# Kernel tuning notes

Measured on AMD Instinct MI355X. Metric: run time of the kernel, lower is better.

Reference implementation:

```python
import jax, jax.numpy as jnp
import numpy as np

B, L, HID, H, FF = 32, 1024, 512, 8, 2048
DH = HID // H  # head_dim = 64; deterministic FAVOR features => M == DH
KEPS = 1e-3    # performer kernel_epsilon
LN_EPS = 1e-6  # flax LayerNorm default


def setup_inputs() -> dict:
    key = jax.random.key(0)
    ks = jax.random.split(key, 12)
    sa = 1.0 / np.sqrt(HID)
    sf = 1.0 / np.sqrt(FF)
    return {
        "x": jax.random.normal(ks[0], (B, L, HID), jnp.float32),
        "Wq": jax.random.normal(ks[1], (HID, H, DH), jnp.float32) * sa,
        "bq": jnp.zeros((H, DH), jnp.float32),
        "Wk": jax.random.normal(ks[2], (HID, H, DH), jnp.float32) * sa,
        "bk": jnp.zeros((H, DH), jnp.float32),
        "Wv": jax.random.normal(ks[3], (HID, H, DH), jnp.float32) * sa,
        "bv": jnp.zeros((H, DH), jnp.float32),
        "Wo": jax.random.normal(ks[4], (H, DH, HID), jnp.float32) * sa,
        "bo": jnp.zeros((HID,), jnp.float32),
        "ln1_scale": jnp.ones((HID,), jnp.float32),
        "ln1_bias": jnp.zeros((HID,), jnp.float32),
        "W1": jax.random.normal(ks[5], (HID, FF), jnp.float32) * sa,
        "b1": jnp.zeros((FF,), jnp.float32),
        "W2": jax.random.normal(ks[6], (FF, HID), jnp.float32) * sf,
        "b2": jnp.zeros((HID,), jnp.float32),
        "ln2_scale": jnp.ones((HID,), jnp.float32),
        "ln2_bias": jnp.zeros((HID,), jnp.float32),
    }


def _layernorm(x, scale, bias):
    mu = jnp.mean(x, axis=-1, keepdims=True)
    var = jnp.mean(jnp.square(x - mu), axis=-1, keepdims=True)
    return (x - mu) * jax.lax.rsqrt(var + LN_EPS) * scale + bias


def _favor_bidirectional(q, k, v):
    # Performer generalized attention, deterministic features:
    # phi(x) = relu(x) + kernel_epsilon, renormalized.
    qp = jax.nn.relu(q) + KEPS  # [B,L,H,M]
    kp = jax.nn.relu(k) + KEPS  # [B,L,H,M]
    kv = jnp.einsum('blhm,blhd->bhmd', kp, v)        # [B,H,M,D]
    num = jnp.einsum('blhm,bhmd->blhd', qp, kv)      # [B,L,H,D]
    den = jnp.einsum('blhm,bhm->blh', qp, kp.sum(axis=1))  # [B,L,H]
    return num / den[..., None]


def reference(x, Wq, bq, Wk, bk, Wv, bv, Wo, bo,
              ln1_scale, ln1_bias, W1, b1, W2, b2, ln2_scale, ln2_bias):
    # Multi-head projections (flax MHA DenseGeneral layout [HID,H,DH])
    q = jnp.einsum('blc,chd->blhd', x, Wq) + bq
    k = jnp.einsum('blc,chd->blhd', x, Wk) + bk
    v = jnp.einsum('blc,chd->blhd', x, Wv) + bv
    attn = _favor_bidirectional(q, k, v)                  # [B,L,H,DH]
    attended = jnp.einsum('blhd,hdc->blc', attn, Wo) + bo # [B,L,HID]
    h = _layernorm(attended + x, ln1_scale, ln1_bias)
    ff = jax.nn.relu(h @ W1 + b1) @ W2 + b2
    return _layernorm(ff + h, ln2_scale, ln2_bias)
```

## Files before the change

kernel.cpp:

```cpp
#include <hip/hip_runtime.h>


#define DI __device__ __forceinline__
#define AS1 __attribute__((address_space(1)))
#define AS3 __attribute__((address_space(3)))
#define GLD16(g, l) __builtin_amdgcn_global_load_lds((const AS1 void*)(g), (AS3 void*)(l), 16, 0, 0)

typedef __attribute__((ext_vector_type(8))) short bf16x8;
typedef __attribute__((ext_vector_type(4))) float f32x4;

DI float b2f(short s){ unsigned int u = ((unsigned int)(unsigned short)s) << 16; float f; __builtin_memcpy(&f, &u, 4); return f; }
DI short f2b(float f){ unsigned int u; __builtin_memcpy(&u, &f, 4); u += 0x7fffu + ((u >> 16) & 1u); return (short)(u >> 16); }

constexpr int Ll = 1024;

__global__ __launch_bounds__(256) void k_cvt_x(const float* __restrict__ x, short* __restrict__ xb){
  long i = (long)blockIdx.x * 256 + threadIdx.x;
  const float4* p = (const float4*)x + i * 2;
  float4 a = p[0], b = p[1];
  bf16x8 o;
  o[0]=f2b(a.x); o[1]=f2b(a.y); o[2]=f2b(a.z); o[3]=f2b(a.w);
  o[4]=f2b(b.x); o[5]=f2b(b.y); o[6]=f2b(b.z); o[7]=f2b(b.w);
  *((bf16x8*)xb + i) = o;
}

__global__ void k_tcvt(const float* __restrict__ in, short* __restrict__ out, int R, int C){
  __shared__ float t[32][33];
  int c0 = blockIdx.x * 32, r0 = blockIdx.y * 32;
  int x = threadIdx.x, y = threadIdx.y;
  #pragma unroll
  for (int j = 0; j < 4; ++j) t[y + 8*j][x] = in[(long)(r0 + y + 8*j) * C + c0 + x];
  __syncthreads();
  #pragma unroll
  for (int j = 0; j < 4; ++j) out[(long)(c0 + y + 8*j) * R + r0 + x] = f2b(t[x][y + 8*j]);
}

__global__ void k_tcvt4(const float* __restrict__ s0, const float* __restrict__ s1,
                        const float* __restrict__ s2, const float* __restrict__ s3,
                        short* __restrict__ d0, short* __restrict__ d1,
                        short* __restrict__ d2, short* __restrict__ d3){
  __shared__ float t[32][33];
  int z = blockIdx.z;
  const float* in = z == 0 ? s0 : z == 1 ? s1 : z == 2 ? s2 : s3;
  short* out      = z == 0 ? d0 : z == 1 ? d1 : z == 2 ? d2 : d3;
  int c0 = blockIdx.x * 32, r0 = blockIdx.y * 32;
  int x = threadIdx.x, y = threadIdx.y;
  #pragma unroll
  for (int j = 0; j < 4; ++j) t[y + 8*j][x] = in[(long)(r0 + y + 8*j) * 512 + c0 + x];
  __syncthreads();
  #pragma unroll
  for (int j = 0; j < 4; ++j) out[(long)(c0 + y + 8*j) * 512 + r0 + x] = f2b(t[x][y + 8*j]);
}

__global__ void k_pack_bias(const float* __restrict__ bq, const float* __restrict__ bk,
                            const float* __restrict__ bv, float* __restrict__ bqkv){
  int i = blockIdx.x * 256 + threadIdx.x;
  if (i < 512) bqkv[i] = bq[i];
  else if (i < 1024) bqkv[i] = bk[i - 512];
  else if (i < 1536) bqkv[i] = bv[i - 1024];
}

template<int EPI, int KD>
__global__ __launch_bounds__(256) void k_gemm(
    const short* __restrict__ A, const short* __restrict__ BT, int NT,
    const float* __restrict__ bias, const float* __restrict__ residF, const short* __restrict__ residB,
    short* __restrict__ oQ, short* __restrict__ oK, short* __restrict__ oV, float* __restrict__ oF)
{
  __shared__ short As[128 * 64];
  __shared__ short Bs[128 * 64];
  const int tid = threadIdx.x;
  const int wave = tid >> 6, lane = tid & 63;
  const int wr = wave >> 1, wc = wave & 1;
  const int lg = lane >> 4, lr = lane & 15;
  const int lrow = lane >> 3;
  const int lslot = (lane & 7) ^ lrow;

  const int per = gridDim.x >> 3;
  const int wg = (blockIdx.x & 7) * per + (blockIdx.x >> 3);
  const long m0 = (long)(wg / NT) * 128, n0 = (long)(wg % NT) * 128;

  f32x4 acc[4][4];
  #pragma unroll
  for (int i = 0; i < 4; ++i)
    #pragma unroll
    for (int j = 0; j < 4; ++j) acc[i][j] = 0.f;

  for (int k0 = 0; k0 < KD; k0 += 64) {
    __syncthreads();
    #pragma unroll
    for (int s = 0; s < 4; ++s) {
      int rs = (s * 4 + wave) * 8;
      GLD16(A  + (m0 + rs + lrow) * KD + k0 + lslot * 8, &As[rs * 64]);
      GLD16(BT + (n0 + rs + lrow) * KD + k0 + lslot * 8, &Bs[rs * 64]);
    }
    __syncthreads();
    #pragma unroll
    for (int kk = 0; kk < 2; ++kk) {
      bf16x8 af[4], bfr[4];
      #pragma unroll
      for (int i = 0; i < 4; ++i) {
        int ra = wr * 64 + i * 16 + lr;
        int rb = wc * 64 + i * 16 + lr;
        af[i]  = *(const bf16x8*)((const char*)As + ra * 128 + ((kk * 64 + lg * 16) ^ ((ra & 7) << 4)));
        bfr[i] = *(const bf16x8*)((const char*)Bs + rb * 128 + ((kk * 64 + lg * 16) ^ ((rb & 7) << 4)));
      }
      #pragma unroll
      for (int i = 0; i < 4; ++i)
        #pragma unroll
        for (int j = 0; j < 4; ++j)
          acc[i][j] = __builtin_amdgcn_mfma_f32_16x16x32_bf16(af[i], bfr[j], acc[i][j], 0, 0, 0);
    }
  }

  #pragma unroll
  for (int i = 0; i < 4; ++i)
    #pragma unroll
    for (int j = 0; j < 4; ++j)
      #pragma unroll
      for (int r = 0; r < 4; ++r) {
        int grow = (int)m0 + wr * 64 + i * 16 + lg * 4 + r;
        int gcol = (int)n0 + wc * 64 + j * 16 + lr;
        float v = acc[i][j][r];
        if constexpr (EPI == 0) {
          v += bias[gcol];
          int which = gcol >> 9, hd = gcol & 511, h = hd >> 6, d = hd & 63;
          int b = grow >> 10, l = grow & 1023;
          long o = ((long)(b * 8 + h) * 1024 + l) * 64 + d;
          if (which == 2) oV[o] = f2b(v);
          else { float p = fmaxf(v, 0.f) + 1e-3f; if (which) oK[o] = f2b(p); else oQ[o] = f2b(p); }
        } else if constexpr (EPI == 1) {
          v += bias[gcol] + residF[(long)grow * 512 + gcol];
          oQ[(long)grow * 512 + gcol] = f2b(v);
        } else if constexpr (EPI == 2) {
          v = fmaxf(v + bias[gcol], 0.f);
          oQ[(long)grow * 2048 + gcol] = f2b(v);
        } else {
          v += bias[gcol] + b2f(residB[(long)grow * 512 + gcol]);
          oF[(long)grow * 512 + gcol] = v;
        }
      }
}

__global__ __launch_bounds__(256) void k_fkv_part(const short* __restrict__ kp, const short* __restrict__ vb,
                                                  float* __restrict__ kvp, float* __restrict__ ksp)
{
  constexpr int LS = 72;
  __shared__ short kps[64 * LS];
  __shared__ short vps[64 * LS];
  int bh = blockIdx.x & 255, c = blockIdx.x >> 8;
  const short* kpp = kp + (long)bh * Ll * 64;
  const short* vpp = vb + (long)bh * Ll * 64;
  int tid = threadIdx.x;
  int mb = (tid & 15) * 4, db = (tid >> 4) * 4;
  float acc[4][4];
  float ks[4] = {0.f, 0.f, 0.f, 0.f};
  #pragma unroll
  for (int i = 0; i < 4; ++i)
    #pragma unroll
    for (int j = 0; j < 4; ++j) acc[i][j] = 0.f;

  for (int l0 = c * 256; l0 < c * 256 + 256; l0 += 64) {
    __syncthreads();
    #pragma unroll
    for (int s = 0; s < 2; ++s) {
      int idx = tid + s * 256;
      int row = idx >> 3, c8 = idx & 7;
      *(bf16x8*)(&kps[row * LS + c8 * 8]) = *(const bf16x8*)(kpp + (long)(l0 + row) * 64 + c8 * 8);
      *(bf16x8*)(&vps[row * LS + c8 * 8]) = *(const bf16x8*)(vpp + (long)(l0 + row) * 64 + c8 * 8);
    }
    __syncthreads();
    #pragma unroll 4
    for (int l = 0; l < 64; ++l) {
      short4 ka = *(const short4*)(&kps[l * LS + mb]);
      short4 va = *(const short4*)(&vps[l * LS + db]);
      float kf[4] = {b2f(ka.x), b2f(ka.y), b2f(ka.z), b2f(ka.w)};
      float vf[4] = {b2f(va.x), b2f(va.y), b2f(va.z), b2f(va.w)};
      if (tid < 16) { ks[0] += kf[0]; ks[1] += kf[1]; ks[2] += kf[2]; ks[3] += kf[3]; }
      #pragma unroll
      for (int i = 0; i < 4; ++i)
        #pragma unroll
        for (int j = 0; j < 4; ++j) acc[i][j] += kf[i] * vf[j];
    }
  }
  float* kout = kvp + (long)c * 1048576 + (long)bh * 4096;
  #pragma unroll
  for (int i = 0; i < 4; ++i)
    #pragma unroll
    for (int j = 0; j < 4; ++j)
      kout[(db + j) * 64 + mb + i] = acc[i][j];
  if (tid < 16) {
    #pragma unroll
    for (int i = 0; i < 4; ++i) ksp[(long)c * 16384 + bh * 64 + mb + i] = ks[i];
  }
}

__global__ __launch_bounds__(256) void k_fkv_reduce(const float* __restrict__ kvp, const float* __restrict__ ksp,
                                                    short* __restrict__ kvt, float* __restrict__ ksum)
{
  int g = blockIdx.x * 256 + threadIdx.x;
  float s = kvp[g] + kvp[g + 1048576] + kvp[g + 2 * 1048576] + kvp[g + 3 * 1048576];
  kvt[g] = f2b(s);
  if (g < 16384)
    ksum[g] = ksp[g] + ksp[g + 16384] + ksp[g + 2 * 16384] + ksp[g + 3 * 16384];
}

__global__ __launch_bounds__(256) void k_favor_num(const short* __restrict__ qp, const short* __restrict__ kvt,
                                                   const float* __restrict__ ksum, short* __restrict__ attn)
{
  constexpr int LS = 72;
  __shared__ short Qs[128 * 64];
  __shared__ short kvs[64 * LS];
  __shared__ float part[256];
  __shared__ float den[128];
  int bh = blockIdx.x >> 3, lt = blockIdx.x & 7;
  int b = bh >> 3, h = bh & 7;
  const short* qpp = qp + ((long)bh * Ll + lt * 128) * 64;
  int tid = threadIdx.x;
  int wave = tid >> 6, lane = tid & 63;
  int lrow = lane >> 3, lslot = (lane & 7) ^ lrow;

  #pragma unroll
  for (int s = 0; s < 4; ++s) {
    int rs = (s * 4 + wave) * 8;
    GLD16(qpp + (long)(rs + lrow) * 64 + lslot * 8, &Qs[rs * 64]);
  }
  #pragma unroll
  for (int s = 0; s < 2; ++s) {
    int idx = tid + s * 256;
    int row = idx >> 3, c8 = idx & 7;
    *(bf16x8*)(&kvs[row * LS + c8 * 8]) = *(const bf16x8*)(kvt + (long)bh * 4096 + row * 64 + c8 * 8);
  }
  __syncthreads();
  {
    int r = tid >> 1, half = tid & 1;
    const float* kss = ksum + bh * 64 + half * 32;
    float s = 0.f;
    #pragma unroll
    for (int c = 0; c < 4; ++c) {
      int cc = half * 4 + c;
      bf16x8 v = *(const bf16x8*)((const char*)Qs + r * 128 + ((cc * 16) ^ ((r & 7) << 4)));
      #pragma unroll
      for (int j = 0; j < 8; ++j) s += b2f(v[j]) * kss[c * 8 + j];
    }
    part[tid] = s;
  }
  __syncthreads();
  if (tid < 128) den[tid] = part[2 * tid] + part[2 * tid + 1];
  __syncthreads();

  int wr = wave >> 1, wc = wave & 1;
  int lg = lane >> 4, lr = lane & 15;
  f32x4 acc[4][2];
  #pragma unroll
  for (int i = 0; i < 4; ++i) { acc[i][0] = 0.f; acc[i][1] = 0.f; }
  #pragma unroll
  for (int kk = 0; kk < 2; ++kk) {
    bf16x8 af[4], bfr[2];
    #pragma unroll
    for (int i = 0; i < 4; ++i) {
      int ra = wr * 64 + i * 16 + lr;
      af[i] = *(const bf16x8*)((const char*)Qs + ra * 128 + ((kk * 64 + lg * 16) ^ ((ra & 7) << 4)));
    }
    #pragma unroll
    for (int j = 0; j < 2; ++j)
      bfr[j] = *(const bf16x8*)(&kvs[(wc * 32 + j * 16 + lr) * LS + kk * 32 + lg * 8]);
    #pragma unroll
    for (int i = 0; i < 4; ++i)
      #pragma unroll
      for (int j = 0; j < 2; ++j)
        acc[i][j] = __builtin_amdgcn_mfma_f32_16x16x32_bf16(af[i], bfr[j], acc[i][j], 0, 0, 0);
  }
  #pragma unroll
  for (int i = 0; i < 4; ++i)
    #pragma unroll
    for (int j = 0; j < 2; ++j)
      #pragma unroll
      for (int r = 0; r < 4; ++r) {
        int rl = wr * 64 + i * 16 + lg * 4 + r;
        int d  = wc * 32 + j * 16 + lr;
        int t  = b * Ll + lt * 128 + rl;
        attn[(long)t * 512 + h * 64 + d] = f2b(acc[i][j][r] / den[rl]);
      }
}

__global__ __launch_bounds__(256) void k_ln_bb(const short* __restrict__ in, const float* __restrict__ sc,
                                               const float* __restrict__ bi, short* __restrict__ ob)
{
  int row = blockIdx.x * 4 + (threadIdx.x >> 6);
  int lane = threadIdx.x & 63;
  bf16x8 v = *((const bf16x8*)(in + (long)row * 512) + lane);
  float e[8];
  #pragma unroll
  for (int j = 0; j < 8; ++j) e[j] = b2f(v[j]);
  float s = 0.f, s2 = 0.f;
  #pragma unroll
  for (int j = 0; j < 8; ++j) { s += e[j]; s2 += e[j] * e[j]; }
  #pragma unroll
  for (int off = 32; off; off >>= 1) { s += __shfl_xor(s, off); s2 += __shfl_xor(s2, off); }
  float mu = s * (1.f / 512.f);
  float var = s2 * (1.f / 512.f) - mu * mu;
  float rstd = rsqrtf(var + 1e-6f);
  int c0 = lane * 8;
  bf16x8 o;
  #pragma unroll
  for (int j = 0; j < 8; ++j) o[j] = f2b((e[j] - mu) * rstd * sc[c0 + j] + bi[c0 + j]);
  *((bf16x8*)(ob + (long)row * 512) + lane) = o;
}

__global__ __launch_bounds__(256) void k_ln_ff(const float* __restrict__ in, const float* __restrict__ sc,
                                               const float* __restrict__ bi, float* __restrict__ of)
{
  int row = blockIdx.x * 4 + (threadIdx.x >> 6);
  int lane = threadIdx.x & 63;
  const float* r = in + (long)row * 512;
  float4 a = *(const float4*)(r + lane * 4);
  float4 b = *(const float4*)(r + 256 + lane * 4);
  float s  = a.x + a.y + a.z + a.w + b.x + b.y + b.z + b.w;
  float s2 = a.x*a.x + a.y*a.y + a.z*a.z + a.w*a.w + b.x*b.x + b.y*b.y + b.z*b.z + b.w*b.w;
  #pragma unroll
  for (int off = 32; off; off >>= 1) { s += __shfl_xor(s, off); s2 += __shfl_xor(s2, off); }
  float mu = s * (1.f / 512.f);
  float var = s2 * (1.f / 512.f) - mu * mu;
  float rstd = rsqrtf(var + 1e-6f);
  int c0 = lane * 4;
  const float* ap = &a.x; const float* bp = &b.x;
  float o0[4], o1[4];
  #pragma unroll
  for (int j = 0; j < 4; ++j) {
    o0[j] = (ap[j] - mu) * rstd * sc[c0 + j]       + bi[c0 + j];
    o1[j] = (bp[j] - mu) * rstd * sc[256 + c0 + j] + bi[256 + c0 + j];
  }
  *(float4*)(of + (long)row * 512 + c0)       = (float4){o0[0], o0[1], o0[2], o0[3]};
  *(float4*)(of + (long)row * 512 + 256 + c0) = (float4){o1[0], o1[1], o1[2], o1[3]};
}

extern "C" void kernel_launch(void* const* d_in, const int* in_sizes, int n_in,
                              void* d_out, int out_size, void* d_ws, size_t ws_size,
                              hipStream_t stream)
{
  const float* x   = (const float*)d_in[0];
  const float* Wq  = (const float*)d_in[1];
  const float* bq  = (const float*)d_in[2];
  const float* Wk  = (const float*)d_in[3];
  const float* bk  = (const float*)d_in[4];
  const float* Wv  = (const float*)d_in[5];
  const float* bv  = (const float*)d_in[6];
  const float* Wo  = (const float*)d_in[7];
  const float* bo  = (const float*)d_in[8];
  const float* g1  = (const float*)d_in[9];
  const float* be1 = (const float*)d_in[10];
  const float* W1  = (const float*)d_in[11];
  const float* b1  = (const float*)d_in[12];
  const float* W2  = (const float*)d_in[13];
  const float* b2  = (const float*)d_in[14];
  const float* g2  = (const float*)d_in[15];
  const float* be2 = (const float*)d_in[16];
  float* out = (float*)d_out;

  const long MB = 1024L * 1024L;
  char* ws = (char*)d_ws;
  short* qp    = (short*)(ws + 0 * MB);
  short* kp    = (short*)(ws + 32 * MB);
  short* vb    = (short*)(ws + 64 * MB);
  short* attn  = (short*)(ws + 32 * MB);
  short* hb    = (short*)(ws + 0 * MB);
  short* hpreB = (short*)(ws + 64 * MB);
  short* ffa   = (short*)(ws + 32 * MB);
  short* wqkvT = (short*)(ws + 96 * MB);
  short* woT   = (short*)(ws + 98 * MB);
  short* w1T   = (short*)(ws + 99 * MB);
  short* w2T   = (short*)(ws + 101 * MB);
  short* kvt   = (short*)(ws + 103 * MB);
  float* ksum  = (float*)(ws + 105 * MB);
  float* bqkv  = (float*)(ws + 105 * MB + 65536);

  short* xb  = (short*)d_out;
  float* kvp = (float*)((char*)d_out + 32 * MB);
  float* ksp = (float*)((char*)d_out + 48 * MB);

  dim3 tb(32, 8);
  k_cvt_x<<<8192, 256, 0, stream>>>(x, xb);
  k_tcvt4<<<dim3(16, 16, 4), tb, 0, stream>>>(Wq, Wk, Wv, Wo,
      wqkvT, wqkvT + 512 * 512, wqkvT + 1024 * 512, woT);
  k_tcvt<<<dim3(64, 16), tb, 0, stream>>>(W1, w1T, 512, 2048);
  k_tcvt<<<dim3(16, 64), tb, 0, stream>>>(W2, w2T, 2048, 512);
  k_pack_bias<<<6, 256, 0, stream>>>(bq, bk, bv, bqkv);

  k_gemm<0, 512><<<3072, 256, 0, stream>>>(xb, wqkvT, 12, bqkv, nullptr, nullptr, qp, kp, vb, nullptr);
  k_fkv_part<<<1024, 256, 0, stream>>>(kp, vb, kvp, ksp);
  k_fkv_reduce<<<4096, 256, 0, stream>>>(kvp, ksp, kvt, ksum);
  k_favor_num<<<2048, 256, 0, stream>>>(qp, kvt, ksum, attn);
  k_gemm<1, 512><<<1024, 256, 0, stream>>>(attn, woT, 4, bo, x, nullptr, hpreB, nullptr, nullptr, nullptr);
  k_ln_bb<<<8192, 256, 0, stream>>>(hpreB, g1, be1, hb);
  for (int c = 0; c < 2; ++c) {
    const short* hbc = hb + (long)c * 16384 * 512;
    k_gemm<2, 512><<<2048, 256, 0, stream>>>(hbc, w1T, 16, b1, nullptr, nullptr, ffa, nullptr, nullptr, nullptr);
    k_gemm<3, 2048><<<512, 256, 0, stream>>>(ffa, w2T, 4, b2, nullptr, hbc, nullptr, nullptr, nullptr, out + (long)c * 16384 * 512);
  }
  k_ln_ff<<<8192, 256, 0, stream>>>(out, g2, be2, out);
}
```

Baseline: 430.7 us.

## Use 256x256 double-buffered GEMM tiles and merge FFN chunks into single launches

Result: faster. 365.9 us (-15.0%).

```diff
diff --git a/kernel.cpp b/kernel.cpp
--- a/kernel.cpp
+++ b/kernel.cpp
@@ -13,6 +13,7 @@
 DI short f2b(float f){ unsigned int u; __builtin_memcpy(&u, &f, 4); u += 0x7fffu + ((u >> 16) & 1u); return (short)(u >> 16); }
 
 constexpr int Ll = 1024;
+constexpr int SPLIT = 16384;
 
 __global__ __launch_bounds__(256) void k_cvt_x(const float* __restrict__ x, short* __restrict__ xb){
   long i = (long)blockIdx.x * 256 + threadIdx.x;
@@ -61,66 +62,102 @@
 }
 
 template<int EPI, int KD>
-__global__ __launch_bounds__(256) void k_gemm(
-    const short* __restrict__ A, const short* __restrict__ BT, int NT,
-    const float* __restrict__ bias, const float* __restrict__ residF, const short* __restrict__ residB,
-    short* __restrict__ oQ, short* __restrict__ oK, short* __restrict__ oV, float* __restrict__ oF)
-{
-  __shared__ short As[128 * 64];
-  __shared__ short Bs[128 * 64];
+__global__ __launch_bounds__(512, 2) void k_gemm256(
+    const short* __restrict__ A0, const short* __restrict__ A1,
+    const short* __restrict__ BT, int NT,
+    const float* __restrict__ bias, const float* __restrict__ residF,
+    short* __restrict__ oQ, short* __restrict__ oK, short* __restrict__ oV,
+    short* __restrict__ o1)
+{
+  __shared__ short lds[65536];
   const int tid = threadIdx.x;
-  const int wave = tid >> 6, lane = tid & 63;
-  const int wr = wave >> 1, wc = wave & 1;
+  const int w = tid >> 6, lane = tid & 63;
+  const int wm = w >> 2, wn = w & 3;
   const int lg = lane >> 4, lr = lane & 15;
-  const int lrow = lane >> 3;
-  const int lslot = (lane & 7) ^ lrow;
+  const int lrow = lane >> 3, lslot = (lane & 7) ^ lrow;
 
   const int per = gridDim.x >> 3;
   const int wg = (blockIdx.x & 7) * per + (blockIdx.x >> 3);
-  const long m0 = (long)(wg / NT) * 128, n0 = (long)(wg % NT) * 128;
-
-  f32x4 acc[4][4];
-  #pragma unroll
-  for (int i = 0; i < 4; ++i)
+  const long m0 = (long)(wg / NT) * 256, n0 = (long)(wg % NT) * 256;
+
+  const short* Ause = A0;
+  long mbase = m0;
+  if (A1 != A0 && m0 >= SPLIT) { Ause = A1; mbase = m0 - SPLIT; }
+
+  f32x4 acc[8][4];
+  #pragma unroll
+  for (int i = 0; i < 8; ++i)
     #pragma unroll
     for (int j = 0; j < 4; ++j) acc[i][j] = 0.f;
 
-  for (int k0 = 0; k0 < KD; k0 += 64) {
+  auto stage_all = [&](int buf, int k0){
+    #pragma unroll
+    for (int half = 0; half < 2; ++half)
+      #pragma unroll
+      for (int q = 0; q < 2; ++q) {
+        int r = w * 16 + q * 8;
+        GLD16(Ause + (mbase + half * 128 + r + lrow) * KD + k0 + lslot * 8,
+              (char*)lds + (buf * 16384 + half * 8192 + r * 64) * 2);
+        GLD16(BT + (n0 + half * 128 + r + lrow) * KD + k0 + lslot * 8,
+              (char*)lds + (32768 + buf * 16384 + half * 8192 + r * 64) * 2);
+      }
+  };
+
+  constexpr int NKT = KD / 64;
+  stage_all(0, 0);
+
+  for (int kt = 0; kt < NKT; ++kt) {
+    const int cur = kt & 1;
     __syncthreads();
-    #pragma unroll
-    for (int s = 0; s < 4; ++s) {
-      int rs = (s * 4 + wave) * 8;
-      GLD16(A  + (m0 + rs + lrow) * KD + k0 + lslot * 8, &As[rs * 64]);
-      GLD16(BT + (n0 + rs + lrow) * KD + k0 + lslot * 8, &Bs[rs * 64]);
-    }
-    __syncthreads();
-    #pragma unroll
-    for (int kk = 0; kk < 2; ++kk) {
-      bf16x8 af[4], bfr[4];
-      #pragma unroll
-      for (int i = 0; i < 4; ++i) {
-        int ra = wr * 64 + i * 16 + lr;
-        int rb = wc * 64 + i * 16 + lr;
-        af[i]  = *(const bf16x8*)((const char*)As + ra * 128 + ((kk * 64 + lg * 16) ^ ((ra & 7) << 4)));
-        bfr[i] = *(const bf16x8*)((const char*)Bs + rb * 128 + ((kk * 64 + lg * 16) ^ ((rb & 7) << 4)));
-      }
+    if (kt + 1 < NKT) stage_all(cur ^ 1, (kt + 1) * 64);
+
+    const char* Ab = (const char*)lds + (cur * 16384 + wm * 8192) * 2;
+    const char* Bb = (const char*)lds + (32768 + cur * 16384 + (wn >> 1) * 8192) * 2;
+
+    bf16x8 fB[2][2][2];
+    #pragma unroll
+    for (int qc = 0; qc < 2; ++qc)
+      #pragma unroll
+      for (int j = 0; j < 2; ++j)
+        #pragma unroll
+        for (int kk = 0; kk < 2; ++kk) {
+          int rb = (wn & 1) * 64 + qc * 32 + j * 16 + lr;
+          fB[qc][j][kk] = *(const bf16x8*)(Bb + rb * 128 + ((kk * 64 + lg * 16) ^ ((rb & 7) << 4)));
+        }
+    #pragma unroll
+    for (int qr = 0; qr < 2; ++qr) {
+      bf16x8 fA[4][2];
       #pragma unroll
       for (int i = 0; i < 4; ++i)
         #pragma unroll
-        for (int j = 0; j < 4; ++j)
-          acc[i][j] = __builtin_amdgcn_mfma_f32_16x16x32_bf16(af[i], bfr[j], acc[i][j], 0, 0, 0);
+        for (int kk = 0; kk < 2; ++kk) {
+          int ra = qr * 64 + i * 16 + lr;
+          fA[i][kk] = *(const bf16x8*)(Ab + ra * 128 + ((kk * 64 + lg * 16) ^ ((ra & 7) << 4)));
+        }
+      __builtin_amdgcn_s_setprio(1);
+      #pragma unroll
+      for (int i = 0; i < 4; ++i)
+        #pragma unroll
+        for (int qc = 0; qc < 2; ++qc)
+          #pragma unroll
+          for (int j = 0; j < 2; ++j)
+            #pragma unroll
+            for (int kk = 0; kk < 2; ++kk)
+              acc[qr * 4 + i][qc * 2 + j] =
+                __builtin_amdgcn_mfma_f32_16x16x32_bf16(fA[i][kk], fB[qc][j][kk], acc[qr * 4 + i][qc * 2 + j], 0, 0, 0);
+      __builtin_amdgcn_s_setprio(0);
     }
   }
 
   #pragma unroll
-  for (int i = 0; i < 4; ++i)
-    #pragma unroll
-    for (int j = 0; j < 4; ++j)
+  for (int fr = 0; fr < 8; ++fr)
+    #pragma unroll
+    for (int fc = 0; fc < 4; ++fc)
       #pragma unroll
       for (int r = 0; r < 4; ++r) {
-        int grow = (int)m0 + wr * 64 + i * 16 + lg * 4 + r;
-        int gcol = (int)n0 + wc * 64 + j * 16 + lr;
-        float v = acc[i][j][r];
+        int grow = (int)m0 + wm * 128 + fr * 16 + lg * 4 + r;
+        int gcol = (int)n0 + wn * 64 + fc * 16 + lr;
+        float v = acc[fr][fc][r];
         if constexpr (EPI == 0) {
           v += bias[gcol];
           int which = gcol >> 9, hd = gcol & 511, h = hd >> 6, d = hd & 63;
@@ -133,10 +170,12 @@
           oQ[(long)grow * 512 + gcol] = f2b(v);
         } else if constexpr (EPI == 2) {
           v = fmaxf(v + bias[gcol], 0.f);
-          oQ[(long)grow * 2048 + gcol] = f2b(v);
+          if (grow < SPLIT) oQ[(long)grow * 2048 + gcol] = f2b(v);
+          else              o1[(long)(grow - SPLIT) * 2048 + gcol] = f2b(v);
         } else {
-          v += bias[gcol] + b2f(residB[(long)grow * 512 + gcol]);
-          oF[(long)grow * 512 + gcol] = v;
+          long idx = (long)grow * 512 + gcol;
+          v += bias[gcol] + b2f(oQ[idx]);
+          oQ[idx] = f2b(v);
         }
       }
 }
@@ -307,31 +346,32 @@
   *((bf16x8*)(ob + (long)row * 512) + lane) = o;
 }
 
-__global__ __launch_bounds__(256) void k_ln_ff(const float* __restrict__ in, const float* __restrict__ sc,
+__global__ __launch_bounds__(256) void k_ln_bf(const short* __restrict__ in, const float* __restrict__ sc,
                                                const float* __restrict__ bi, float* __restrict__ of)
 {
   int row = blockIdx.x * 4 + (threadIdx.x >> 6);
   int lane = threadIdx.x & 63;
-  const float* r = in + (long)row * 512;
-  float4 a = *(const float4*)(r + lane * 4);
-  float4 b = *(const float4*)(r + 256 + lane * 4);
-  float s  = a.x + a.y + a.z + a.w + b.x + b.y + b.z + b.w;
-  float s2 = a.x*a.x + a.y*a.y + a.z*a.z + a.w*a.w + b.x*b.x + b.y*b.y + b.z*b.z + b.w*b.w;
+  bf16x8 v = *((const bf16x8*)(in + (long)row * 512) + lane);
+  float e[8];
+  #pragma unroll
+  for (int j = 0; j < 8; ++j) e[j] = b2f(v[j]);
+  float s = 0.f, s2 = 0.f;
+  #pragma unroll
+  for (int j = 0; j < 8; ++j) { s += e[j]; s2 += e[j] * e[j]; }
   #pragma unroll
   for (int off = 32; off; off >>= 1) { s += __shfl_xor(s, off); s2 += __shfl_xor(s2, off); }
   float mu = s * (1.f / 512.f);
   float var = s2 * (1.f / 512.f) - mu * mu;
   float rstd = rsqrtf(var + 1e-6f);
-  int c0 = lane * 4;
-  const float* ap = &a.x; const float* bp = &b.x;
+  int c0 = lane * 8;
   float o0[4], o1[4];
   #pragma unroll
   for (int j = 0; j < 4; ++j) {
-    o0[j] = (ap[j] - mu) * rstd * sc[c0 + j]       + bi[c0 + j];
-    o1[j] = (bp[j] - mu) * rstd * sc[256 + c0 + j] + bi[256 + c0 + j];
-  }
-  *(float4*)(of + (long)row * 512 + c0)       = (float4){o0[0], o0[1], o0[2], o0[3]};
-  *(float4*)(of + (long)row * 512 + 256 + c0) = (float4){o1[0], o1[1], o1[2], o1[3]};
+    o0[j] = (e[j]     - mu) * rstd * sc[c0 + j]     + bi[c0 + j];
+    o1[j] = (e[4 + j] - mu) * rstd * sc[c0 + 4 + j] + bi[c0 + 4 + j];
+  }
+  *(float4*)(of + (long)row * 512 + c0)     = (float4){o0[0], o0[1], o0[2], o0[3]};
+  *(float4*)(of + (long)row * 512 + c0 + 4) = (float4){o1[0], o1[1], o1[2], o1[3]};
 }
 
 extern "C" void kernel_launch(void* const* d_in, const int* in_sizes, int n_in,
@@ -365,7 +405,7 @@
   short* attn  = (short*)(ws + 32 * MB);
   short* hb    = (short*)(ws + 0 * MB);
   short* hpreB = (short*)(ws + 64 * MB);
-  short* ffa   = (short*)(ws + 32 * MB);
+  short* ffa0  = (short*)(ws + 32 * MB);
   short* wqkvT = (short*)(ws + 96 * MB);
   short* woT   = (short*)(ws + 98 * MB);
   short* w1T   = (short*)(ws + 99 * MB);
@@ -374,9 +414,10 @@
   float* ksum  = (float*)(ws + 105 * MB);
   float* bqkv  = (float*)(ws + 105 * MB + 65536);
 
-  short* xb  = (short*)d_out;
-  float* kvp = (float*)((char*)d_out + 32 * MB);
-  float* ksp = (float*)((char*)d_out + 48 * MB);
+  short* xb   = (short*)d_out;
+  float* kvp  = (float*)((char*)d_out + 32 * MB);
+  float* ksp  = (float*)((char*)d_out + 48 * MB);
+  short* ffa1 = (short*)d_out;
 
   dim3 tb(32, 8);
   k_cvt_x<<<8192, 256, 0, stream>>>(x, xb);
@@ -386,16 +427,13 @@
   k_tcvt<<<dim3(16, 64), tb, 0, stream>>>(W2, w2T, 2048, 512);
   k_pack_bias<<<6, 256, 0, stream>>>(bq, bk, bv, bqkv);
 
-  k_gemm<0, 512><<<3072, 256, 0, stream>>>(xb, wqkvT, 12, bqkv, nullptr, nullptr, qp, kp, vb, nullptr);
+  k_gemm256<0, 512><<<768, 512, 0, stream>>>(xb, xb, wqkvT, 6, bqkv, nullptr, qp, kp, vb, nullptr);
   k_fkv_part<<<1024, 256, 0, stream>>>(kp, vb, kvp, ksp);
   k_fkv_reduce<<<4096, 256, 0, stream>>>(kvp, ksp, kvt, ksum);
   k_favor_num<<<2048, 256, 0, stream>>>(qp, kvt, ksum, attn);
-  k_gemm<1, 512><<<1024, 256, 0, stream>>>(attn, woT, 4, bo, x, nullptr, hpreB, nullptr, nullptr, nullptr);
+  k_gemm256<1, 512><<<256, 512, 0, stream>>>(attn, attn, woT, 2, bo, x, hpreB, nullptr, nullptr, nullptr);
   k_ln_bb<<<8192, 256, 0, stream>>>(hpreB, g1, be1, hb);
-  for (int c = 0; c < 2; ++c) {
-    const short* hbc = hb + (long)c * 16384 * 512;
-    k_gemm<2, 512><<<2048, 256, 0, stream>>>(hbc, w1T, 16, b1, nullptr, nullptr, ffa, nullptr, nullptr, nullptr);
-    k_gemm<3, 2048><<<512, 256, 0, stream>>>(ffa, w2T, 4, b2, nullptr, hbc, nullptr, nullptr, nullptr, out + (long)c * 16384 * 512);
-  }
-  k_ln_ff<<<8192, 256, 0, stream>>>(out, g2, be2, out);
-}
+  k_gemm256<2, 512><<<1024, 512, 0, stream>>>(hb, hb, w1T, 8, b1, nullptr, ffa0, nullptr, nullptr, ffa1);
+  k_gemm256<3, 2048><<<256, 512, 0, stream>>>(ffa0, ffa1, w2T, 2, b2, nullptr, hb, nullptr, nullptr, nullptr);
+  k_ln_bf<<<8192, 256, 0, stream>>>(hb, g2, be2, out);
+}
```
